# Kernel tuning notes

Hardware: AMD Instinct MI355X
Metric: run time of the kernel (lower is better)

The kernel has to match this reference:

```python
import math
import jax, jax.numpy as jnp
import numpy as np

D_MODEL = 1024
SEQ_LEN = 8192
EMB_DIM = 3
ORDER = 16
BATCH = 4


def _make_pos_emb_z(seq_len, emb_dim):
    # PositionalEmbedding.__init__: t, complex-exponential bands (real+imag)
    t = np.linspace(0.0, 1.0, seq_len)[None, :, None]                      # (1, L, 1)
    bands = (emb_dim - 1) // 2                                             # = 1
    t_rescaled = np.linspace(0.0, seq_len - 1, seq_len)[None, :, None]
    w = 2 * math.pi * t_rescaled / seq_len                                 # (1, L, 1)
    f = np.linspace(1e-4, bands - 1, bands)[None, None]                    # (1, 1, bands)
    zc = np.exp(-1j * f * w)                                               # (1, L, bands)
    z = np.concatenate([t, zc.real, zc.imag], axis=-1)                     # (1, L, emb_dim)
    return jnp.asarray(z, dtype=jnp.float32)


def setup_inputs() -> dict:
    key = jax.random.key(0)
    ks = jax.random.split(key, 12)
    s_in = 1.0 / math.sqrt(EMB_DIM)
    s_h = 1.0 / math.sqrt(ORDER)
    return {
        "x": jax.random.normal(ks[0], (BATCH, D_MODEL, SEQ_LEN), dtype=jnp.float32),
        "L": SEQ_LEN,
        "z": _make_pos_emb_z(SEQ_LEN, EMB_DIM),                            # learnable pos emb
        "W1": jax.random.uniform(ks[1], (EMB_DIM, ORDER), minval=-s_in, maxval=s_in),
        "b1": jax.random.uniform(ks[2], (ORDER,), minval=-s_in, maxval=s_in),
        "W2": jax.random.uniform(ks[3], (ORDER, ORDER), minval=-s_h, maxval=s_h),
        "b2": jax.random.uniform(ks[4], (ORDER,), minval=-s_h, maxval=s_h),
        "W3": jax.random.uniform(ks[5], (ORDER, ORDER), minval=-s_h, maxval=s_h),
        "b3": jax.random.uniform(ks[6], (ORDER,), minval=-s_h, maxval=s_h),
        "Wout": jax.random.uniform(ks[7], (ORDER, D_MODEL), minval=-s_h, maxval=s_h),
        "freq": jnp.ones((1, ORDER), dtype=jnp.float32),                   # Sin freq, w=1 (shared act)
        "bias": jax.random.normal(ks[8], (D_MODEL,), dtype=jnp.float32),
    }


def _hyena_forward(x, L, z, W1, b1, W2, b2, W3, b3, Wout, freq, bias):
    # ---- implicit filter MLP (tiny) ----
    zz = z[:, :L]                                                          # (1, L, emb_dim)
    h = jnp.sin(freq * (zz @ W1 + b1))
    h = jnp.sin(freq * (h @ W2 + b2))
    h = jnp.sin(freq * (h @ W3 + b3))
    h = h @ Wout                                                           # (1, L, D)
    # ---- exponential modulation ----
    t = jnp.linspace(0.0, 1.0, SEQ_LEN, dtype=jnp.float32)[None, :, None][:, :L]
    max_decay = math.log(0.01) / 0.3
    min_decay = math.log(0.01) / 1.5
    deltas = jnp.linspace(min_decay, max_decay, D_MODEL, dtype=jnp.float32)[None, None]
    h = h * jnp.exp(-t * jnp.abs(deltas))                                  # (1, L, D)
    k = h[0].T.astype(jnp.float32)                                         # (D, L)
    # ---- FFT-based causal long convolution (safari fftconv) ----
    n = 2 * L
    xf = jnp.fft.rfft(x.astype(jnp.float32), n=n)                          # (B, D, n//2+1) complex
    kf = jnp.fft.rfft(k, n=n)                                              # (D, n//2+1)
    y = jnp.fft.irfft(xf * kf, n=n)[..., :L]                               # (B, D, L)
    return y + x * bias[:, None]


def reference(x, L, z, W1, b1, W2, b2, W3, b3, Wout, freq, bias):
    return _hyena_forward(x, L, z, W1, b1, W2, b2, W3, b3, Wout, freq, bias)
```

## Files before the change

kernel.cpp:

```cpp
#include <hip/hip_runtime.h>

#define NT 512
#define SEQ_LEN 8192

static __device__ __forceinline__ float2 f2(float x, float y){ return make_float2(x,y); }
static __device__ __forceinline__ float2 cadd(float2 a, float2 b){ return f2(a.x+b.x, a.y+b.y); }
static __device__ __forceinline__ float2 csub(float2 a, float2 b){ return f2(a.x-b.x, a.y-b.y); }
static __device__ __forceinline__ float2 cmul(float2 a, float2 b){ return f2(a.x*b.x-a.y*b.y, a.x*b.y+a.y*b.x); }
static __device__ __forceinline__ float2 cmulc(float2 a, float2 b){ return f2(a.x*b.x+a.y*b.y, a.y*b.x-a.x*b.y); }
static __device__ __forceinline__ float2 mul_mi(float2 a){ return f2(a.y, -a.x); }
static __device__ __forceinline__ float2 mul_pi(float2 a){ return f2(-a.y, a.x); }
static __device__ __forceinline__ int swz(int e){ return e ^ ((e>>4)&15) ^ ((e>>8)&15); }
static __device__ __forceinline__ int rev13(int v){ return (int)(__brev((unsigned)v) >> 19); }

__global__ void hyena_mlp(const float* __restrict__ z,
                          const float* __restrict__ W1, const float* __restrict__ b1,
                          const float* __restrict__ W2, const float* __restrict__ b2,
                          const float* __restrict__ W3, const float* __restrict__ b3,
                          const float* __restrict__ freq,
                          float* __restrict__ h3) {
    int j = blockIdx.x * blockDim.x + threadIdx.x;
    if (j >= SEQ_LEN) return;
    float z0 = z[3*j+0], z1 = z[3*j+1], z2 = z[3*j+2];
    float ha[16], hb[16];
#pragma unroll
    for (int o = 0; o < 16; ++o) {
        float acc = b1[o] + z0*W1[o] + z1*W1[16+o] + z2*W1[32+o];
        ha[o] = sinf(freq[o] * acc);
    }
#pragma unroll
    for (int p = 0; p < 16; ++p) {
        float acc = b2[p];
#pragma unroll
        for (int o = 0; o < 16; ++o) acc += ha[o] * W2[o*16+p];
        hb[p] = sinf(freq[p] * acc);
    }
#pragma unroll
    for (int q = 0; q < 16; ++q) {
        float acc = b3[q];
#pragma unroll
        for (int o = 0; o < 16; ++o) acc += hb[o] * W3[o*16+q];
        h3[j*16+q] = sinf(freq[q] * acc);
    }
}

#define PJ 128
__global__ void hyena_proj(const float* __restrict__ h3, const float* __restrict__ Wout,
                           float* __restrict__ krows) {
    __shared__ float sW[16][1024];
    __shared__ float sh[PJ][17];
    const int t = threadIdx.x;
    const int jb = blockIdx.x * PJ;
    for (int i = t; i < 16*1024; i += 256) sW[i>>10][i&1023] = Wout[i];
    for (int i = t; i < PJ*16; i += 256)   sh[i>>4][i&15]    = h3[(size_t)(jb + (i>>4))*16 + (i&15)];
    __syncthreads();
    const float dmin = -3.0701134573253941f;
    const float dmax = -15.350567286626971f;
    const int jloc = t & 127;
    const int dloc = t >> 7;
    const float tj = (float)(jb + jloc) * (1.0f/8191.0f);
#pragma unroll 1
    for (int db = 0; db < 1024; db += 2) {
        int d = db + dloc;
        float absd = fabsf(dmin + (dmax - dmin) * ((float)d * (1.0f/1023.0f)));
        float acc = 0.f;
#pragma unroll
        for (int o = 0; o < 16; ++o) acc += sh[jloc][o] * sW[o][d];
        krows[(size_t)d*SEQ_LEN + jb + jloc] = acc * __expf(-tj * absd);
    }
}

static __device__ __forceinline__ void dif3(float2 r[8], float2 wd){
    const float2 c2 = f2(0.7071067811865476f,-0.7071067811865476f);
    float2 wd2 = cmul(wd,wd), wd4 = cmul(wd2,wd2);
    float2 wc2 = cmul(wd,c2);
    { float2 u=r[0], v=r[4]; r[0]=cadd(u,v); r[4]=cmul(csub(u,v), wd); }
    { float2 u=r[1], v=r[5]; r[1]=cadd(u,v); r[5]=cmul(csub(u,v), wc2); }
    { float2 u=r[2], v=r[6]; r[2]=cadd(u,v); r[6]=mul_mi(cmul(csub(u,v), wd)); }
    { float2 u=r[3], v=r[7]; r[3]=cadd(u,v); r[7]=mul_mi(cmul(csub(u,v), wc2)); }
    { float2 u=r[0], v=r[2]; r[0]=cadd(u,v); r[2]=cmul(csub(u,v), wd2); }
    { float2 u=r[1], v=r[3]; r[1]=cadd(u,v); r[3]=mul_mi(cmul(csub(u,v), wd2)); }
    { float2 u=r[4], v=r[6]; r[4]=cadd(u,v); r[6]=cmul(csub(u,v), wd2); }
    { float2 u=r[5], v=r[7]; r[5]=cadd(u,v); r[7]=mul_mi(cmul(csub(u,v), wd2)); }
    { float2 u=r[0], v=r[1]; r[0]=cadd(u,v); r[1]=cmul(csub(u,v), wd4); }
    { float2 u=r[2], v=r[3]; r[2]=cadd(u,v); r[3]=cmul(csub(u,v), wd4); }
    { float2 u=r[4], v=r[5]; r[4]=cadd(u,v); r[5]=cmul(csub(u,v), wd4); }
    { float2 u=r[6], v=r[7]; r[6]=cadd(u,v); r[7]=cmul(csub(u,v), wd4); }
}
static __device__ __forceinline__ void dit3(float2 r[8], float2 wd){
    const float2 c2 = f2(0.7071067811865476f,-0.7071067811865476f);
    float2 wd2 = cmul(wd,wd), wd4 = cmul(wd2,wd2);
    float2 wc2 = cmul(wd,c2);
    { float2 u=r[0]; float2 t=cmulc(r[1], wd4); r[0]=cadd(u,t); r[1]=csub(u,t); }
    { float2 u=r[2]; float2 t=cmulc(r[3], wd4); r[2]=cadd(u,t); r[3]=csub(u,t); }
    { float2 u=r[4]; float2 t=cmulc(r[5], wd4); r[4]=cadd(u,t); r[5]=csub(u,t); }
    { float2 u=r[6]; float2 t=cmulc(r[7], wd4); r[6]=cadd(u,t); r[7]=csub(u,t); }
    { float2 u=r[0]; float2 t=cmulc(r[2], wd2);         r[0]=cadd(u,t); r[2]=csub(u,t); }
    { float2 u=r[1]; float2 t=mul_pi(cmulc(r[3], wd2)); r[1]=cadd(u,t); r[3]=csub(u,t); }
    { float2 u=r[4]; float2 t=cmulc(r[6], wd2);         r[4]=cadd(u,t); r[6]=csub(u,t); }
    { float2 u=r[5]; float2 t=mul_pi(cmulc(r[7], wd2)); r[5]=cadd(u,t); r[7]=csub(u,t); }
    { float2 u=r[0]; float2 t=cmulc(r[4], wd);          r[0]=cadd(u,t); r[4]=csub(u,t); }
    { float2 u=r[1]; float2 t=cmulc(r[5], wc2);         r[1]=cadd(u,t); r[5]=csub(u,t); }
    { float2 u=r[2]; float2 t=mul_pi(cmulc(r[6], wd));  r[2]=cadd(u,t); r[6]=csub(u,t); }
    { float2 u=r[3]; float2 t=mul_pi(cmulc(r[7], wc2)); r[3]=cadd(u,t); r[7]=csub(u,t); }
}

static __device__ __forceinline__ void readpair(const float2* cv, int p, float2& e0, float2& e1){
    int sp = swz(p);
    float4 q = *(const float4*)&cv[sp & ~1];
    float2 lo = f2(q.x,q.y), hi = f2(q.z,q.w);
    if (sp & 1) { e0 = hi; e1 = lo; } else { e0 = lo; e1 = hi; }
}
static __device__ __forceinline__ void writepair(float2* cv, int p, float2 e0, float2 e1){
    int sp = swz(p);
    float4 q;
    if (sp & 1) q = make_float4(e1.x,e1.y,e0.x,e0.y);
    else        q = make_float4(e0.x,e0.y,e1.x,e1.y);
    *(float4*)&cv[sp & ~1] = q;
}

static __device__ __forceinline__ float2 getw(const float2* T1, const float2* T2, int k){
    return cmul(T1[k>>6], T2[k&63]);
}
static __device__ __forceinline__ float4 kpack(float2 Ck, float2 Cm, float2 w, float bds){
    const float s = 1.0f/16384.0f;
    float2 A  = f2(0.5f*(Ck.x+Cm.x), 0.5f*(Ck.y-Cm.y));
    float2 Bc = f2(0.5f*(Ck.x-Cm.x), 0.5f*(Ck.y+Cm.y));
    float2 B  = f2(Bc.y, -Bc.x);
    float2 wB = cmul(w, B);
    return make_float4((A.x+wB.x)*s + bds, (A.y+wB.y)*s,
                       (A.x-wB.x)*s + bds, -((A.y-wB.y)*s));
}
static __device__ __forceinline__ void pwmul(float2 Ck, float2 Cm, float4 Kp, float2 w,
                                             float2& Dk, float2& Dm){
    float2 A  = f2(0.5f*(Ck.x+Cm.x), 0.5f*(Ck.y-Cm.y));
    float2 Bc = f2(0.5f*(Ck.x-Cm.x), 0.5f*(Ck.y+Cm.y));
    float2 B  = f2(Bc.y, -Bc.x);
    float2 wB = cmul(w, B);
    float2 Xk = f2(A.x+wB.x, A.y+wB.y);
    float2 Xm = f2(A.x-wB.x, -(A.y-wB.y));
    float2 Yk = cmul(Xk, f2(Kp.x,Kp.y));
    float2 Ym = cmul(Xm, f2(Kp.z,Kp.w));
    float2 A2 = f2(Yk.x+Ym.x, Yk.y-Ym.y);
    float2 Bt = f2(Yk.x-Ym.x, Yk.y+Ym.y);
    float2 B2 = cmulc(Bt, w);
    Dk = f2(A2.x - B2.y, A2.y + B2.x);
    Dm = f2(A2.x + B2.y, B2.x - A2.y);
}

#define SMEM_BYTES (9348 * 8)

template<bool USE_K>
__global__ __launch_bounds__(NT, 2)
void hyena_conv(const float* __restrict__ h3g, const float* __restrict__ Wout,
                const float* __restrict__ krows,
                const float* __restrict__ x, const float* __restrict__ bias,
                float* __restrict__ out) {
    extern __shared__ float2 smem[];
    float2* cv  = smem;
    float2* tab = cv + 8192;
    float2* T1  = tab + 1024;
    float2* T2  = T1 + 64;
    float2* Kex = T2 + 64;
    const int t = threadIdx.x;
    const int d = blockIdx.x;
    const float PI = 3.14159265358979323846f;

#pragma unroll
    for (int i = 0; i < 2; ++i) {
        int p = t + 512*i;
        float s_,c_; sincosf((PI/4096.0f)*(float)p, &s_, &c_); tab[p] = f2(c_, -s_);
    }
    if (t < 64)       { float s_,c_; sincosf((PI/128.0f)*(float)t, &s_,&c_); T1[t] = f2(c_,-s_); }
    else if (t < 128) { int l=t-64; float s_,c_; sincosf((PI/8192.0f)*(float)l,&s_,&c_); T2[l] = f2(c_,-s_); }
    __syncthreads();

    const float2 wdB = tab[(t&127)<<3];
    const float2 wdC = tab[(t&15)<<6];
    const float2 wdD = tab[(t&1)<<9];

    const float bds = bias[d] * (1.0f/16384.0f);

    float2 r[8];
#pragma unroll 1
    for (int gi = 0; gi < 2; ++gi) {
        int g = t + 512*gi;
        if (USE_K) {
            const float2* kr = (const float2*)(krows + (size_t)d * SEQ_LEN);
#pragma unroll
            for (int k = 0; k < 4; ++k) r[k] = kr[g + 1024*k];
        } else {
            const float dmin = -3.0701134573253941f;
            const float dmax = -15.350567286626971f;
            const float absd = fabsf(dmin + (dmax - dmin) * ((float)d * (1.0f/1023.0f)));
#pragma unroll
            for (int k = 0; k < 4; ++k) {
                int e = g + 1024*k;
                const float4* h4 = (const float4*)(h3g + (size_t)(2*e)*16);
                float a0 = 0.f, a1 = 0.f;
#pragma unroll
                for (int v4 = 0; v4 < 4; ++v4) {
                    float4 q0 = h4[v4], q1 = h4[4+v4];
                    float w0 = Wout[(4*v4+0)*1024 + d], w1 = Wout[(4*v4+1)*1024 + d];
                    float w2 = Wout[(4*v4+2)*1024 + d], w3 = Wout[(4*v4+3)*1024 + d];
                    a0 += q0.x*w0 + q0.y*w1 + q0.z*w2 + q0.w*w3;
                    a1 += q1.x*w0 + q1.y*w1 + q1.z*w2 + q1.w*w3;
                }
                float ta = (float)(2*e)   * (1.0f/8191.0f);
                float tb = (float)(2*e+1) * (1.0f/8191.0f);
                r[k] = f2(a0 * __expf(-ta*absd), a1 * __expf(-tb*absd));
            }
        }
#pragma unroll
        for (int k = 4; k < 8; ++k) r[k] = f2(0.f, 0.f);
        dif3(r, tab[g]);
#pragma unroll
        for (int k = 0; k < 8; ++k) cv[swz(g + 1024*k)] = r[k];
    }
    __syncthreads();
#pragma unroll 1
    for (int gi = 0; gi < 2; ++gi) {
        int g = t + 512*gi;
        int base = ((g>>7)<<10) | (g&127);
#pragma unroll
        for (int k = 0; k < 8; ++k) r[k] = cv[swz(base + 128*k)];
        dif3(r, wdB);
#pragma unroll
        for (int k = 0; k < 8; ++k) cv[swz(base + 128*k)] = r[k];
    }
    __syncthreads();
#pragma unroll 1
    for (int gi = 0; gi < 2; ++gi) {
        int g = t + 512*gi;
        int base = ((g>>4)<<7) | (g&15);
#pragma unroll
        for (int k = 0; k < 8; ++k) r[k] = cv[swz(base + 16*k)];
        dif3(r, wdC);
#pragma unroll
        for (int k = 0; k < 8; ++k) cv[swz(base + 16*k)] = r[k];
    }
    __syncthreads();
#pragma unroll 1
    for (int gi = 0; gi < 2; ++gi) {
        int g = t + 512*gi;
        int base = ((g>>1)<<4) | (g&1);
#pragma unroll
        for (int k = 0; k < 8; ++k) r[k] = cv[swz(base + 2*k)];
        dif3(r, wdD);
#pragma unroll
        for (int k = 0; k < 8; ++k) cv[swz(base + 2*k)] = r[k];
    }
    __syncthreads();

    float4 Ka[4], Kb[4];
#pragma unroll
    for (int q = 0; q < 4; ++q) {
        int f = t + 512*q;
        if (f == 0) {
            float2 a0,a1; readpair(cv, 0, a0, a1);
            float2 C0 = cadd(a0,a1), C4 = csub(a0,a1);
            const float s = 1.0f/16384.0f;
            Ka[q] = make_float4((C0.x+C0.y)*s + bds, (C0.x-C0.y)*s + bds, C4.x*s + bds, -C4.y*s);
            Kb[q] = make_float4(0.f,0.f,0.f,0.f);
        } else {
            int g = 4096 - f;
            float2 a0,a1,b0,b1;
            readpair(cv, rev13(f), a0, a1);
            readpair(cv, rev13(g), b0, b1);
            float2 Cf=cadd(a0,a1), Cf4=csub(a0,a1), Cg=cadd(b0,b1), Cg4=csub(b0,b1);
            Ka[q] = kpack(Cf, Cg4, getw(T1,T2,f), bds);
            Kb[q] = kpack(Cg, Cf4, getw(T1,T2,g), bds);
        }
    }
    if (t == 0) {
        float2 b0,b1; readpair(cv, 2, b0, b1);
        float4 K20 = kpack(cadd(b0,b1), csub(b0,b1), getw(T1,T2,2048), bds);
        Kex[0] = f2(K20.x, K20.y);
        Kex[1] = f2(K20.z, K20.w);
    }
    __syncthreads();

#pragma unroll 1
    for (int b = 0; b < 4; ++b) {
        const float2* xr = (const float2*)(x + ((size_t)b*1024 + d)*SEQ_LEN);
        float2* yr = (float2*)(out + ((size_t)b*1024 + d)*SEQ_LEN);

#pragma unroll 1
        for (int gi = 0; gi < 2; ++gi) {
            int g = t + 512*gi;
#pragma unroll
            for (int k = 0; k < 4; ++k) r[k] = xr[g + 1024*k];
#pragma unroll
            for (int k = 4; k < 8; ++k) r[k] = f2(0.f,0.f);
            dif3(r, tab[g]);
#pragma unroll
            for (int k = 0; k < 8; ++k) cv[swz(g + 1024*k)] = r[k];
        }
        __syncthreads();
#pragma unroll 1
        for (int gi = 0; gi < 2; ++gi) {
            int g = t + 512*gi;
            int base = ((g>>7)<<10) | (g&127);
#pragma unroll
            for (int k = 0; k < 8; ++k) r[k] = cv[swz(base + 128*k)];
            dif3(r, wdB);
#pragma unroll
            for (int k = 0; k < 8; ++k) cv[swz(base + 128*k)] = r[k];
        }
        __syncthreads();
#pragma unroll 1
        for (int gi = 0; gi < 2; ++gi) {
            int g = t + 512*gi;
            int base = ((g>>4)<<7) | (g&15);
#pragma unroll
            for (int k = 0; k < 8; ++k) r[k] = cv[swz(base + 16*k)];
            dif3(r, wdC);
#pragma unroll
            for (int k = 0; k < 8; ++k) cv[swz(base + 16*k)] = r[k];
        }
        __syncthreads();
#pragma unroll 1
        for (int gi = 0; gi < 2; ++gi) {
            int g = t + 512*gi;
            int base = ((g>>1)<<4) | (g&1);
#pragma unroll
            for (int k = 0; k < 8; ++k) r[k] = cv[swz(base + 2*k)];
            dif3(r, wdD);
#pragma unroll
            for (int k = 0; k < 8; ++k) cv[swz(base + 2*k)] = r[k];
        }
        __syncthreads();

#pragma unroll
        for (int q = 0; q < 4; ++q) {
            int f = t + 512*q;
            if (f == 0) {
                float2 a0,a1; readpair(cv, 0, a0, a1);
                float2 C0 = cadd(a0,a1), C4 = csub(a0,a1);
                float R0 = C0.x + C0.y, RN = C0.x - C0.y;
                float Y0 = R0 * Ka[0].x, YN = RN * Ka[0].y;
                float2 D0 = f2(Y0+YN, Y0-YN);
                float2 Y4 = cmul(f2(C4.x,-C4.y), f2(Ka[0].z, Ka[0].w));
                float2 D4 = f2(2.f*Y4.x, -2.f*Y4.y);
                writepair(cv, 0, cadd(D0,D4), csub(D0,D4));
            } else {
                int g = 4096 - f;
                int p1 = rev13(f), p2 = rev13(g);
                float2 a0,a1,b0,b1;
                readpair(cv, p1, a0, a1);
                readpair(cv, p2, b0, b1);
                float2 Cf=cadd(a0,a1), Cf4=csub(a0,a1), Cg=cadd(b0,b1), Cg4=csub(b0,b1);
                float2 Df,Dg4,Dg,Df4;
                pwmul(Cf, Cg4, Ka[q], getw(T1,T2,f), Df, Dg4);
                pwmul(Cg, Cf4, Kb[q], getw(T1,T2,g), Dg, Df4);
                writepair(cv, p1, cadd(Df,Df4), csub(Df,Df4));
                writepair(cv, p2, cadd(Dg,Dg4), csub(Dg,Dg4));
            }
        }
        if (t == 0) {
            float4 K20 = make_float4(Kex[0].x, Kex[0].y, Kex[1].x, Kex[1].y);
            float2 b0,b1; readpair(cv, 2, b0, b1);
            float2 Ck=cadd(b0,b1), Cm=csub(b0,b1), Dk, Dm;
            pwmul(Ck, Cm, K20, getw(T1,T2,2048), Dk, Dm);
            writepair(cv, 2, cadd(Dk,Dm), csub(Dk,Dm));
        }
        __syncthreads();

#pragma unroll 1
        for (int gi = 0; gi < 2; ++gi) {
            int g = t + 512*gi;
            int base = ((g>>1)<<4) | (g&1);
#pragma unroll
            for (int k = 0; k < 8; ++k) r[k] = cv[swz(base + 2*k)];
            dit3(r, wdD);
#pragma unroll
            for (int k = 0; k < 8; ++k) cv[swz(base + 2*k)] = r[k];
        }
        __syncthreads();
#pragma unroll 1
        for (int gi = 0; gi < 2; ++gi) {
            int g = t + 512*gi;
            int base = ((g>>4)<<7) | (g&15);
#pragma unroll
            for (int k = 0; k < 8; ++k) r[k] = cv[swz(base + 16*k)];
            dit3(r, wdC);
#pragma unroll
            for (int k = 0; k < 8; ++k) cv[swz(base + 16*k)] = r[k];
        }
        __syncthreads();
#pragma unroll 1
        for (int gi = 0; gi < 2; ++gi) {
            int g = t + 512*gi;
            int base = ((g>>7)<<10) | (g&127);
#pragma unroll
            for (int k = 0; k < 8; ++k) r[k] = cv[swz(base + 128*k)];
            dit3(r, wdB);
#pragma unroll
            for (int k = 0; k < 8; ++k) cv[swz(base + 128*k)] = r[k];
        }
        __syncthreads();
#pragma unroll 1
        for (int gi = 0; gi < 2; ++gi) {
            int g = t + 512*gi;
#pragma unroll
            for (int k = 0; k < 8; ++k) r[k] = cv[swz(g + 1024*k)];
            dit3(r, tab[g]);
#pragma unroll
            for (int k = 0; k < 4; ++k) yr[g + 1024*k] = r[k];
        }
        __syncthreads();
    }
}

extern "C" void kernel_launch(void* const* d_in, const int* in_sizes, int n_in,
                              void* d_out, int out_size, void* d_ws, size_t ws_size,
                              hipStream_t stream) {
    const float* x    = (const float*)d_in[0];
    const float* z    = (const float*)d_in[2];
    const float* W1   = (const float*)d_in[3];
    const float* b1   = (const float*)d_in[4];
    const float* W2   = (const float*)d_in[5];
    const float* b2   = (const float*)d_in[6];
    const float* W3   = (const float*)d_in[7];
    const float* b3   = (const float*)d_in[8];
    const float* Wout = (const float*)d_in[9];
    const float* freq = (const float*)d_in[10];
    const float* bias = (const float*)d_in[11];
    float* out = (float*)d_out;
    float* h3  = (float*)d_ws;
    float* krows = (float*)((char*)d_ws + 512*1024);

    const size_t need = 512*1024 + (size_t)32*1024*1024;
    const bool use_k = ws_size >= need;

    hipLaunchKernelGGL(hyena_mlp, dim3(SEQ_LEN/256), dim3(256), 0, stream,
                       z, W1, b1, W2, b2, W3, b3, freq, h3);

    static bool attr_set = false;
    if (!attr_set) {
        (void)hipFuncSetAttribute((const void*)hyena_conv<true>,
                                  hipFuncAttributeMaxDynamicSharedMemorySize, SMEM_BYTES);
        (void)hipFuncSetAttribute((const void*)hyena_conv<false>,
                                  hipFuncAttributeMaxDynamicSharedMemorySize, SMEM_BYTES);
        attr_set = true;
    }

    if (use_k) {
        hipLaunchKernelGGL(hyena_proj, dim3(SEQ_LEN/PJ), dim3(256), 0, stream,
                           h3, Wout, krows);
        hipLaunchKernelGGL(hyena_conv<true>, dim3(1024), dim3(NT), SMEM_BYTES, stream,
                           h3, Wout, krows, x, bias, out);
    } else {
        hipLaunchKernelGGL(hyena_conv<false>, dim3(1024), dim3(NT), SMEM_BYTES, stream,
                           h3, Wout, krows, x, bias, out);
    }
}
```

Measured before the change: 356.9 us.

## Split filter spectrum into separate kernel; radix-16 FFT processing two batches per block

Adds a kernel that computes the filter's FFT spectrum once per channel and stores packed coefficients in workspace. A new convolution kernel reads these, then runs radix-16 FFT passes (three stages instead of four radix-8) on two batch rows at once with double shared buffers and one block per CU. This removes the per-block filter FFT and halves the barrier count per row. In exchange it uses more registers, shared memory and workspace (64 MB), and occupancy drops to one block.

```diff
diff --git a/kernel.cpp b/kernel.cpp
--- a/kernel.cpp
+++ b/kernel.cpp
@@ -68,6 +68,67 @@
         for (int o = 0; o < 16; ++o) acc += sh[jloc][o] * sW[o][d];
         krows[(size_t)d*SEQ_LEN + jb + jloc] = acc * __expf(-tj * absd);
     }
+}
+
+static __device__ __forceinline__ void dif4(float2 r[16], float2 wd){
+    const float2 c1 = f2(0.9238795325112867f,-0.3826834323650898f);
+    const float2 c2 = f2(0.7071067811865476f,-0.7071067811865476f);
+    const float2 c3 = f2(0.3826834323650898f,-0.9238795325112867f);
+    float2 wc = cmul(wd,wd), wb = cmul(wc,wc), wa = cmul(wb,wb);
+    float2 t0 = wd, t1 = cmul(wd,c1), t2 = cmul(wd,c2), t3 = cmul(wd,c3);
+    float2 u0 = wc, u1 = cmul(wc,c2);
+    { float2 u=r[0], v=r[8];  r[0]=cadd(u,v); r[8] =cmul(csub(u,v), t0); }
+    { float2 u=r[1], v=r[9];  r[1]=cadd(u,v); r[9] =cmul(csub(u,v), t1); }
+    { float2 u=r[2], v=r[10]; r[2]=cadd(u,v); r[10]=cmul(csub(u,v), t2); }
+    { float2 u=r[3], v=r[11]; r[3]=cadd(u,v); r[11]=cmul(csub(u,v), t3); }
+    { float2 u=r[4], v=r[12]; r[4]=cadd(u,v); r[12]=mul_mi(cmul(csub(u,v), t0)); }
+    { float2 u=r[5], v=r[13]; r[5]=cadd(u,v); r[13]=mul_mi(cmul(csub(u,v), t1)); }
+    { float2 u=r[6], v=r[14]; r[6]=cadd(u,v); r[14]=mul_mi(cmul(csub(u,v), t2)); }
+    { float2 u=r[7], v=r[15]; r[7]=cadd(u,v); r[15]=mul_mi(cmul(csub(u,v), t3)); }
+#pragma unroll
+    for (int b = 0; b < 16; b += 8) {
+        { float2 u=r[b+0], v=r[b+4]; r[b+0]=cadd(u,v); r[b+4]=cmul(csub(u,v), u0); }
+        { float2 u=r[b+1], v=r[b+5]; r[b+1]=cadd(u,v); r[b+5]=cmul(csub(u,v), u1); }
+        { float2 u=r[b+2], v=r[b+6]; r[b+2]=cadd(u,v); r[b+6]=mul_mi(cmul(csub(u,v), u0)); }
+        { float2 u=r[b+3], v=r[b+7]; r[b+3]=cadd(u,v); r[b+7]=mul_mi(cmul(csub(u,v), u1)); }
+    }
+#pragma unroll
+    for (int b = 0; b < 16; b += 4) {
+        { float2 u=r[b+0], v=r[b+2]; r[b+0]=cadd(u,v); r[b+2]=cmul(csub(u,v), wb); }
+        { float2 u=r[b+1], v=r[b+3]; r[b+1]=cadd(u,v); r[b+3]=mul_mi(cmul(csub(u,v), wb)); }
+    }
+#pragma unroll
+    for (int b = 0; b < 16; b += 2) { float2 u=r[b], v=r[b+1]; r[b]=cadd(u,v); r[b+1]=cmul(csub(u,v), wa); }
+}
+static __device__ __forceinline__ void dit4(float2 r[16], float2 wd){
+    const float2 c1 = f2(0.9238795325112867f,-0.3826834323650898f);
+    const float2 c2 = f2(0.7071067811865476f,-0.7071067811865476f);
+    const float2 c3 = f2(0.3826834323650898f,-0.9238795325112867f);
+    float2 wc = cmul(wd,wd), wb = cmul(wc,wc), wa = cmul(wb,wb);
+    float2 t0 = wd, t1 = cmul(wd,c1), t2 = cmul(wd,c2), t3 = cmul(wd,c3);
+    float2 u0 = wc, u1 = cmul(wc,c2);
+#pragma unroll
+    for (int b = 0; b < 16; b += 2) { float2 u=r[b]; float2 t=cmulc(r[b+1], wa); r[b]=cadd(u,t); r[b+1]=csub(u,t); }
+#pragma unroll
+    for (int b = 0; b < 16; b += 4) {
+        { float2 u=r[b+0]; float2 t=cmulc(r[b+2], wb);         r[b+0]=cadd(u,t); r[b+2]=csub(u,t); }
+        { float2 u=r[b+1]; float2 t=mul_pi(cmulc(r[b+3], wb)); r[b+1]=cadd(u,t); r[b+3]=csub(u,t); }
+    }
+#pragma unroll
+    for (int b = 0; b < 16; b += 8) {
+        { float2 u=r[b+0]; float2 t=cmulc(r[b+4], u0);         r[b+0]=cadd(u,t); r[b+4]=csub(u,t); }
+        { float2 u=r[b+1]; float2 t=cmulc(r[b+5], u1);         r[b+1]=cadd(u,t); r[b+5]=csub(u,t); }
+        { float2 u=r[b+2]; float2 t=mul_pi(cmulc(r[b+6], u0)); r[b+2]=cadd(u,t); r[b+6]=csub(u,t); }
+        { float2 u=r[b+3]; float2 t=mul_pi(cmulc(r[b+7], u1)); r[b+3]=cadd(u,t); r[b+7]=csub(u,t); }
+    }
+    { float2 u=r[0]; float2 t=cmulc(r[8],  t0);        r[0]=cadd(u,t); r[8] =csub(u,t); }
+    { float2 u=r[1]; float2 t=cmulc(r[9],  t1);        r[1]=cadd(u,t); r[9] =csub(u,t); }
+    { float2 u=r[2]; float2 t=cmulc(r[10], t2);        r[2]=cadd(u,t); r[10]=csub(u,t); }
+    { float2 u=r[3]; float2 t=cmulc(r[11], t3);        r[3]=cadd(u,t); r[11]=csub(u,t); }
+    { float2 u=r[4]; float2 t=mul_pi(cmulc(r[12], t0)); r[4]=cadd(u,t); r[12]=csub(u,t); }
+    { float2 u=r[5]; float2 t=mul_pi(cmulc(r[13], t1)); r[5]=cadd(u,t); r[13]=csub(u,t); }
+    { float2 u=r[6]; float2 t=mul_pi(cmulc(r[14], t2)); r[6]=cadd(u,t); r[14]=csub(u,t); }
+    { float2 u=r[7]; float2 t=mul_pi(cmulc(r[15], t3)); r[7]=cadd(u,t); r[15]=csub(u,t); }
 }
 
 static __device__ __forceinline__ void dif3(float2 r[8], float2 wd){
@@ -148,14 +209,254 @@
     Dm = f2(A2.x + B2.y, B2.x - A2.y);
 }
 
-#define SMEM_BYTES (9348 * 8)
-
+#define SMEMK_BYTES (8832 * 8)
+__global__ __launch_bounds__(NT)
+void hyena_kspec(const float* __restrict__ h3g, const float* __restrict__ Wout,
+                 const float* __restrict__ bias, float4* __restrict__ A) {
+    extern __shared__ float2 smem[];
+    float2* cv  = smem;
+    float2* tab = cv + 8192;
+    float2* T1  = tab + 512;
+    float2* T2  = T1 + 64;
+    const int t = threadIdx.x;
+    const int d = blockIdx.x;
+    const float PI = 3.14159265358979323846f;
+
+    { float s_,c_; sincosf((PI/4096.0f)*(float)t, &s_, &c_); tab[t] = f2(c_, -s_); }
+    if (t < 64)       { float s_,c_; sincosf((PI/128.0f)*(float)t, &s_,&c_); T1[t] = f2(c_,-s_); }
+    else if (t < 128) { int l=t-64; float s_,c_; sincosf((PI/8192.0f)*(float)l,&s_,&c_); T2[l] = f2(c_,-s_); }
+    __syncthreads();
+
+    const float2 wd1 = tab[t];
+    const float2 wd2 = tab[(t&31)<<4];
+    const float2 wd3 = tab[(t&1)<<8];
+    const int b2 = ((t>>5)<<9) | (t&31);
+    const int b3 = ((t>>1)<<5) | (t&1);
+
+    const float dmin = -3.0701134573253941f;
+    const float dmax = -15.350567286626971f;
+    const float absd = fabsf(dmin + (dmax - dmin) * ((float)d * (1.0f/1023.0f)));
+    const float bds = bias[d] * (1.0f/16384.0f);
+
+    float2 r[16];
+    {
+        float wcol[16];
+#pragma unroll
+        for (int o = 0; o < 16; ++o) wcol[o] = Wout[o*1024 + d];
+#pragma unroll
+        for (int k = 0; k < 8; ++k) {
+            int e = t + 512*k;
+            const float4* h4 = (const float4*)(h3g + (size_t)(2*e)*16);
+            float a0 = 0.f, a1 = 0.f;
+#pragma unroll
+            for (int v4 = 0; v4 < 4; ++v4) {
+                float4 q0 = h4[v4], q1 = h4[4+v4];
+                a0 += q0.x*wcol[4*v4] + q0.y*wcol[4*v4+1] + q0.z*wcol[4*v4+2] + q0.w*wcol[4*v4+3];
+                a1 += q1.x*wcol[4*v4] + q1.y*wcol[4*v4+1] + q1.z*wcol[4*v4+2] + q1.w*wcol[4*v4+3];
+            }
+            float ta = (float)(2*e)   * (1.0f/8191.0f);
+            float tb = (float)(2*e+1) * (1.0f/8191.0f);
+            r[k] = f2(a0 * __expf(-ta*absd), a1 * __expf(-tb*absd));
+        }
+    }
+#pragma unroll
+    for (int k = 8; k < 16; ++k) r[k] = f2(0.f, 0.f);
+
+    dif4(r, wd1);
+#pragma unroll
+    for (int k = 0; k < 16; ++k) cv[swz(t + 512*k)] = r[k];
+    __syncthreads();
+#pragma unroll
+    for (int k = 0; k < 16; ++k) r[k] = cv[swz(b2 + 32*k)];
+    dif4(r, wd2);
+#pragma unroll
+    for (int k = 0; k < 16; ++k) cv[swz(b2 + 32*k)] = r[k];
+    __syncthreads();
+#pragma unroll
+    for (int k = 0; k < 16; ++k) r[k] = cv[swz(b3 + 2*k)];
+    dif4(r, wd3);
+#pragma unroll
+    for (int k = 0; k < 16; ++k) cv[swz(b3 + 2*k)] = r[k];
+    __syncthreads();
+
+    float4* Ad = A + (size_t)d * 4096;
+#pragma unroll 1
+    for (int q = 0; q < 4; ++q) {
+        int f = t + 512*q;
+        if (f == 0) {
+            float2 a0,a1; readpair(cv, 0, a0, a1);
+            float2 C0 = cadd(a0,a1), C4 = csub(a0,a1);
+            const float s = 1.0f/16384.0f;
+            Ad[0] = make_float4((C0.x+C0.y)*s + bds, (C0.x-C0.y)*s + bds, C4.x*s + bds, -C4.y*s);
+        } else {
+            int g = 4096 - f;
+            float2 a0,a1,b0,b1;
+            readpair(cv, rev13(f), a0, a1);
+            readpair(cv, rev13(g), b0, b1);
+            float2 Cf=cadd(a0,a1), Cf4=csub(a0,a1), Cg=cadd(b0,b1), Cg4=csub(b0,b1);
+            Ad[f] = kpack(Cf, Cg4, getw(T1,T2,f), bds);
+            Ad[g] = kpack(Cg, Cf4, getw(T1,T2,g), bds);
+        }
+    }
+    if (t == 0) {
+        float2 b0,b1; readpair(cv, 2, b0, b1);
+        Ad[2048] = kpack(cadd(b0,b1), csub(b0,b1), getw(T1,T2,2048), bds);
+    }
+}
+
+#define SMEM2_BYTES (17024 * 8)
+__global__ __launch_bounds__(NT, 1)
+void hyena_conv2(const float4* __restrict__ A,
+                 const float* __restrict__ x, float* __restrict__ out) {
+    extern __shared__ float2 smem[];
+    float2* cv0 = smem;
+    float2* cv1 = smem + 8192;
+    float2* tab = smem + 16384;
+    float2* T1  = tab + 512;
+    float2* T2  = T1 + 64;
+    const int t = threadIdx.x;
+    const int d = blockIdx.x;
+    const float PI = 3.14159265358979323846f;
+
+    { float s_,c_; sincosf((PI/4096.0f)*(float)t, &s_, &c_); tab[t] = f2(c_, -s_); }
+    if (t < 64)       { float s_,c_; sincosf((PI/128.0f)*(float)t, &s_,&c_); T1[t] = f2(c_,-s_); }
+    else if (t < 128) { int l=t-64; float s_,c_; sincosf((PI/8192.0f)*(float)l,&s_,&c_); T2[l] = f2(c_,-s_); }
+    __syncthreads();
+
+    const float2 wd1 = tab[t];
+    const float2 wd2 = tab[(t&31)<<4];
+    const float2 wd3 = tab[(t&1)<<8];
+    const int b2 = ((t>>5)<<9) | (t&31);
+    const int b3 = ((t>>1)<<5) | (t&1);
+    const float4* Ad = A + (size_t)d * 4096;
+
+    float2 r[16];
+#pragma unroll 1
+    for (int bp = 0; bp < 2; ++bp) {
+        const float2* xr0 = (const float2*)(x + ((size_t)(2*bp)*1024   + d)*SEQ_LEN);
+        const float2* xr1 = (const float2*)(x + ((size_t)(2*bp+1)*1024 + d)*SEQ_LEN);
+        float2* yr0 = (float2*)(out + ((size_t)(2*bp)*1024   + d)*SEQ_LEN);
+        float2* yr1 = (float2*)(out + ((size_t)(2*bp+1)*1024 + d)*SEQ_LEN);
+
+#pragma unroll 1
+        for (int ci = 0; ci < 2; ++ci) {
+            float2* c = ci ? cv1 : cv0;
+            const float2* xr = ci ? xr1 : xr0;
+#pragma unroll
+            for (int k = 0; k < 8; ++k) r[k] = xr[t + 512*k];
+#pragma unroll
+            for (int k = 8; k < 16; ++k) r[k] = f2(0.f,0.f);
+            dif4(r, wd1);
+#pragma unroll
+            for (int k = 0; k < 16; ++k) c[swz(t + 512*k)] = r[k];
+        }
+        __syncthreads();
+#pragma unroll 1
+        for (int ci = 0; ci < 2; ++ci) {
+            float2* c = ci ? cv1 : cv0;
+#pragma unroll
+            for (int k = 0; k < 16; ++k) r[k] = c[swz(b2 + 32*k)];
+            dif4(r, wd2);
+#pragma unroll
+            for (int k = 0; k < 16; ++k) c[swz(b2 + 32*k)] = r[k];
+        }
+        __syncthreads();
+#pragma unroll 1
+        for (int ci = 0; ci < 2; ++ci) {
+            float2* c = ci ? cv1 : cv0;
+#pragma unroll
+            for (int k = 0; k < 16; ++k) r[k] = c[swz(b3 + 2*k)];
+            dif4(r, wd3);
+#pragma unroll
+            for (int k = 0; k < 16; ++k) c[swz(b3 + 2*k)] = r[k];
+        }
+        __syncthreads();
+
+        {
+            float4 KA_[4], KB_[4];
+#pragma unroll
+            for (int q = 0; q < 4; ++q) {
+                int f = t + 512*q;
+                KA_[q] = Ad[f];
+                KB_[q] = Ad[(f == 0) ? 2048 : (4096 - f)];
+            }
+#pragma unroll 1
+            for (int ci = 0; ci < 2; ++ci) {
+                float2* c = ci ? cv1 : cv0;
+#pragma unroll
+                for (int q = 0; q < 4; ++q) {
+                    int f = t + 512*q;
+                    if (f == 0) {
+                        float2 a0,a1; readpair(c, 0, a0, a1);
+                        float2 C0 = cadd(a0,a1), C4 = csub(a0,a1);
+                        float Y0 = (C0.x+C0.y) * KA_[0].x, YN = (C0.x-C0.y) * KA_[0].y;
+                        float2 D0 = f2(Y0+YN, Y0-YN);
+                        float2 Y4 = cmul(f2(C4.x,-C4.y), f2(KA_[0].z, KA_[0].w));
+                        float2 D4 = f2(2.f*Y4.x, -2.f*Y4.y);
+                        writepair(c, 0, cadd(D0,D4), csub(D0,D4));
+                        float2 q0,q1; readpair(c, 2, q0, q1);
+                        float2 Ck=cadd(q0,q1), Cm=csub(q0,q1), Dk, Dm;
+                        pwmul(Ck, Cm, KB_[0], getw(T1,T2,2048), Dk, Dm);
+                        writepair(c, 2, cadd(Dk,Dm), csub(Dk,Dm));
+                    } else {
+                        int g = 4096 - f;
+                        int p1 = rev13(f), p2 = rev13(g);
+                        float2 a0,a1,b0,b1;
+                        readpair(c, p1, a0, a1);
+                        readpair(c, p2, b0, b1);
+                        float2 Cf=cadd(a0,a1), Cf4=csub(a0,a1), Cg=cadd(b0,b1), Cg4=csub(b0,b1);
+                        float2 Df,Dg4,Dg,Df4;
+                        pwmul(Cf, Cg4, KA_[q], getw(T1,T2,f), Df, Dg4);
+                        pwmul(Cg, Cf4, KB_[q], getw(T1,T2,g), Dg, Df4);
+                        writepair(c, p1, cadd(Df,Df4), csub(Df,Df4));
+                        writepair(c, p2, cadd(Dg,Dg4), csub(Dg,Dg4));
+                    }
+                }
+            }
+        }
+        __syncthreads();
+
+#pragma unroll 1
+        for (int ci = 0; ci < 2; ++ci) {
+            float2* c = ci ? cv1 : cv0;
+#pragma unroll
+            for (int k = 0; k < 16; ++k) r[k] = c[swz(b3 + 2*k)];
+            dit4(r, wd3);
+#pragma unroll
+            for (int k = 0; k < 16; ++k) c[swz(b3 + 2*k)] = r[k];
+        }
+        __syncthreads();
+#pragma unroll 1
+        for (int ci = 0; ci < 2; ++ci) {
+            float2* c = ci ? cv1 : cv0;
+#pragma unroll
+            for (int k = 0; k < 16; ++k) r[k] = c[swz(b2 + 32*k)];
+            dit4(r, wd2);
+#pragma unroll
+            for (int k = 0; k < 16; ++k) c[swz(b2 + 32*k)] = r[k];
+        }
+        __syncthreads();
+#pragma unroll 1
+        for (int ci = 0; ci < 2; ++ci) {
+            float2* c = ci ? cv1 : cv0;
+            float2* yr = ci ? yr1 : yr0;
+#pragma unroll
+            for (int k = 0; k < 16; ++k) r[k] = c[swz(t + 512*k)];
+            dit4(r, wd1);
+#pragma unroll
+            for (int k = 0; k < 8; ++k) yr[t + 512*k] = r[k];
+        }
+        __syncthreads();
+    }
+}
+
+#define SMEMF_BYTES (9348 * 8)
 template<bool USE_K>
 __global__ __launch_bounds__(NT, 2)
-void hyena_conv(const float* __restrict__ h3g, const float* __restrict__ Wout,
-                const float* __restrict__ krows,
-                const float* __restrict__ x, const float* __restrict__ bias,
-                float* __restrict__ out) {
+void hyena_conv_r10(const float* __restrict__ h3g, const float* __restrict__ Wout,
+                    const float* __restrict__ krows,
+                    const float* __restrict__ x, const float* __restrict__ bias,
+                    float* __restrict__ out) {
     extern __shared__ float2 smem[];
     float2* cv  = smem;
     float2* tab = cv + 8192;
@@ -178,7 +479,6 @@
     const float2 wdB = tab[(t&127)<<3];
     const float2 wdC = tab[(t&15)<<6];
     const float2 wdD = tab[(t&1)<<9];
-
     const float bds = bias[d] * (1.0f/16384.0f);
 
     float2 r[8];
@@ -220,8 +520,7 @@
     __syncthreads();
 #pragma unroll 1
     for (int gi = 0; gi < 2; ++gi) {
-        int g = t + 512*gi;
-        int base = ((g>>7)<<10) | (g&127);
+        int g = t + 512*gi; int base = ((g>>7)<<10) | (g&127);
 #pragma unroll
         for (int k = 0; k < 8; ++k) r[k] = cv[swz(base + 128*k)];
         dif3(r, wdB);
@@ -231,8 +530,7 @@
     __syncthreads();
 #pragma unroll 1
     for (int gi = 0; gi < 2; ++gi) {
-        int g = t + 512*gi;
-        int base = ((g>>4)<<7) | (g&15);
+        int g = t + 512*gi; int base = ((g>>4)<<7) | (g&15);
 #pragma unroll
         for (int k = 0; k < 8; ++k) r[k] = cv[swz(base + 16*k)];
         dif3(r, wdC);
@@ -242,8 +540,7 @@
     __syncthreads();
 #pragma unroll 1
     for (int gi = 0; gi < 2; ++gi) {
-        int g = t + 512*gi;
-        int base = ((g>>1)<<4) | (g&1);
+        int g = t + 512*gi; int base = ((g>>1)<<4) | (g&1);
 #pragma unroll
         for (int k = 0; k < 8; ++k) r[k] = cv[swz(base + 2*k)];
         dif3(r, wdD);
@@ -284,7 +581,6 @@
     for (int b = 0; b < 4; ++b) {
         const float2* xr = (const float2*)(x + ((size_t)b*1024 + d)*SEQ_LEN);
         float2* yr = (float2*)(out + ((size_t)b*1024 + d)*SEQ_LEN);
-
 #pragma unroll 1
         for (int gi = 0; gi < 2; ++gi) {
             int g = t + 512*gi;
@@ -299,8 +595,7 @@
         __syncthreads();
 #pragma unroll 1
         for (int gi = 0; gi < 2; ++gi) {
-            int g = t + 512*gi;
-            int base = ((g>>7)<<10) | (g&127);
+            int g = t + 512*gi; int base = ((g>>7)<<10) | (g&127);
 #pragma unroll
             for (int k = 0; k < 8; ++k) r[k] = cv[swz(base + 128*k)];
             dif3(r, wdB);
@@ -310,8 +605,7 @@
         __syncthreads();
 #pragma unroll 1
         for (int gi = 0; gi < 2; ++gi) {
-            int g = t + 512*gi;
-            int base = ((g>>4)<<7) | (g&15);
+            int g = t + 512*gi; int base = ((g>>4)<<7) | (g&15);
 #pragma unroll
             for (int k = 0; k < 8; ++k) r[k] = cv[swz(base + 16*k)];
             dif3(r, wdC);
@@ -321,8 +615,7 @@
         __syncthreads();
 #pragma unroll 1
         for (int gi = 0; gi < 2; ++gi) {
-            int g = t + 512*gi;
-            int base = ((g>>1)<<4) | (g&1);
+            int g = t + 512*gi; int base = ((g>>1)<<4) | (g&1);
 #pragma unroll
             for (int k = 0; k < 8; ++k) r[k] = cv[swz(base + 2*k)];
             dif3(r, wdD);
@@ -330,15 +623,13 @@
             for (int k = 0; k < 8; ++k) cv[swz(base + 2*k)] = r[k];
         }
         __syncthreads();
-
 #pragma unroll
         for (int q = 0; q < 4; ++q) {
             int f = t + 512*q;
             if (f == 0) {
                 float2 a0,a1; readpair(cv, 0, a0, a1);
                 float2 C0 = cadd(a0,a1), C4 = csub(a0,a1);
-                float R0 = C0.x + C0.y, RN = C0.x - C0.y;
-                float Y0 = R0 * Ka[0].x, YN = RN * Ka[0].y;
+                float Y0 = (C0.x+C0.y) * Ka[0].x, YN = (C0.x-C0.y) * Ka[0].y;
                 float2 D0 = f2(Y0+YN, Y0-YN);
                 float2 Y4 = cmul(f2(C4.x,-C4.y), f2(Ka[0].z, Ka[0].w));
                 float2 D4 = f2(2.f*Y4.x, -2.f*Y4.y);
@@ -365,11 +656,9 @@
             writepair(cv, 2, cadd(Dk,Dm), csub(Dk,Dm));
         }
         __syncthreads();
-
 #pragma unroll 1
         for (int gi = 0; gi < 2; ++gi) {
-            int g = t + 512*gi;
-            int base = ((g>>1)<<4) | (g&1);
+            int g = t + 512*gi; int base = ((g>>1)<<4) | (g&1);
 #pragma unroll
             for (int k = 0; k < 8; ++k) r[k] = cv[swz(base + 2*k)];
             dit3(r, wdD);
@@ -379,8 +668,7 @@
         __syncthreads();
 #pragma unroll 1
         for (int gi = 0; gi < 2; ++gi) {
-            int g = t + 512*gi;
-            int base = ((g>>4)<<7) | (g&15);
+            int g = t + 512*gi; int base = ((g>>4)<<7) | (g&15);
 #pragma unroll
             for (int k = 0; k < 8; ++k) r[k] = cv[swz(base + 16*k)];
             dit3(r, wdC);
@@ -390,8 +678,7 @@
         __syncthreads();
 #pragma unroll 1
         for (int gi = 0; gi < 2; ++gi) {
-            int g = t + 512*gi;
-            int base = ((g>>7)<<10) | (g&127);
+            int g = t + 512*gi; int base = ((g>>7)<<10) | (g&127);
 #pragma unroll
             for (int k = 0; k < 8; ++k) r[k] = cv[swz(base + 128*k)];
             dit3(r, wdB);
@@ -428,30 +715,40 @@
     const float* bias = (const float*)d_in[11];
     float* out = (float*)d_out;
     float* h3  = (float*)d_ws;
+    float4* A  = (float4*)((char*)d_ws + 512*1024);
     float* krows = (float*)((char*)d_ws + 512*1024);
 
-    const size_t need = 512*1024 + (size_t)32*1024*1024;
-    const bool use_k = ws_size >= need;
+    const size_t need2 = 512*1024 + (size_t)1024*4096*16;
+    const size_t need1 = 512*1024 + (size_t)32*1024*1024;
 
     hipLaunchKernelGGL(hyena_mlp, dim3(SEQ_LEN/256), dim3(256), 0, stream,
                        z, W1, b1, W2, b2, W3, b3, freq, h3);
 
     static bool attr_set = false;
     if (!attr_set) {
-        (void)hipFuncSetAttribute((const void*)hyena_conv<true>,
-                                  hipFuncAttributeMaxDynamicSharedMemorySize, SMEM_BYTES);
-        (void)hipFuncSetAttribute((const void*)hyena_conv<false>,
-                                  hipFuncAttributeMaxDynamicSharedMemorySize, SMEM_BYTES);
+        (void)hipFuncSetAttribute((const void*)hyena_kspec,
+                                  hipFuncAttributeMaxDynamicSharedMemorySize, SMEMK_BYTES);
+        (void)hipFuncSetAttribute((const void*)hyena_conv2,
+                                  hipFuncAttributeMaxDynamicSharedMemorySize, SMEM2_BYTES);
+        (void)hipFuncSetAttribute((const void*)hyena_conv_r10<true>,
+                                  hipFuncAttributeMaxDynamicSharedMemorySize, SMEMF_BYTES);
+        (void)hipFuncSetAttribute((const void*)hyena_conv_r10<false>,
+                                  hipFuncAttributeMaxDynamicSharedMemorySize, SMEMF_BYTES);
         attr_set = true;
     }
 
-    if (use_k) {
+    if (ws_size >= need2) {
+        hipLaunchKernelGGL(hyena_kspec, dim3(1024), dim3(NT), SMEMK_BYTES, stream,
+                           h3, Wout, bias, A);
+        hipLaunchKernelGGL(hyena_conv2, dim3(1024), dim3(NT), SMEM2_BYTES, stream,
+                           A, x, out);
+    } else if (ws_size >= need1) {
         hipLaunchKernelGGL(hyena_proj, dim3(SEQ_LEN/PJ), dim3(256), 0, stream,
                            h3, Wout, krows);
-        hipLaunchKernelGGL(hyena_conv<true>, dim3(1024), dim3(NT), SMEM_BYTES, stream,
+        hipLaunchKernelGGL(hyena_conv_r10<true>, dim3(1024), dim3(NT), SMEMF_BYTES, stream,
                            h3, Wout, krows, x, bias, out);
     } else {
-        hipLaunchKernelGGL(hyena_conv<false>, dim3(1024), dim3(NT), SMEM_BYTES, stream,
+        hipLaunchKernelGGL(hyena_conv_r10<false>, dim3(1024), dim3(NT), SMEMF_BYTES, stream,
                            h3, Wout, krows, x, bias, out);
     }
 }
```

Result: slower. 582.2 us (+63.1%).
